# Optimization experiments

Hardware: AMD Instinct MI355X
Metric: run time of the kernel (lower is better)

The kernel has to match this reference:

```python
import jax, jax.numpy as jnp
import numpy as np

G, N, K, H, D = 16, 256, 128, 32, 768
NUM_ATOM_TYPES = 128
NUM_EDGE_TYPES = NUM_ATOM_TYPES * NUM_ATOM_TYPES  # 16384
T_STEPS = 1000


def setup_inputs() -> dict:
    key = jax.random.key(0)
    ks = jax.random.split(key, 12)
    return {
        "pos": jax.random.normal(ks[0], (G, N, 3), dtype=jnp.float32) * 3.0,
        "x": jax.random.randint(ks[1], (G, N, 1), 0, NUM_ATOM_TYPES, dtype=jnp.int32),
        "t": jax.random.randint(ks[2], (G,), 0, T_STEPS, dtype=jnp.int32),
        "means": jax.random.uniform(ks[3], (T_STEPS, K), jnp.float32, 0.0, 3.0),
        "stds": jax.random.uniform(ks[4], (T_STEPS, K), jnp.float32, 0.0, 3.0),
        "mul_w": jnp.ones((NUM_EDGE_TYPES, 1), jnp.float32),
        "bias_w": jnp.zeros((NUM_EDGE_TYPES, 1), jnp.float32),
        "w1": jax.random.normal(ks[5], (K, K), jnp.float32) / np.sqrt(K),
        "b1": jnp.zeros((K,), jnp.float32),
        "w2": jax.random.normal(ks[6], (K, H), jnp.float32) / np.sqrt(K),
        "b2": jnp.zeros((H,), jnp.float32),
        "we": jax.random.normal(ks[7], (K, D), jnp.float32) / np.sqrt(K),
        "be": jnp.zeros((D,), jnp.float32),
    }


def _forward(pos, x, t, means, stds, mul_w, bias_w, w1, b1, w2, b2, we, be):
    atoms = x[:, :, 0]  # [G, N]
    edge_types = atoms[:, :, None] * NUM_ATOM_TYPES + atoms[:, None, :]  # [G,N,N]
    pad = atoms == 0  # [G, N]
    pos = jnp.where(pad[..., None], 0.0, pos)
    # delta_pos[g,i,j] = pos[g,j] - pos[g,i]
    delta_pos = pos[:, None, :, :] - pos[:, :, None, :]  # [G,N,N,3]
    sq = jnp.sum(delta_pos * delta_pos, axis=-1)  # [G,N,N]
    dist = jnp.sqrt(jnp.where(sq > 0, sq, 1.0)) * (sq > 0)  # safe norm, grad-safe at 0
    delta_pos = delta_pos / (dist[..., None] + 1e-5)
    # Gaussian basis expansion
    mul = mul_w[edge_types]   # [G,N,N,1]
    bias = bias_w[edge_types]  # [G,N,N,1]
    xg = mul * dist[..., None] + bias  # [G,N,N,1] -> broadcasts to K
    mean = means[t][:, None, None, :]               # [G,1,1,K]
    std = jnp.abs(stds[t])[:, None, None, :] + 1e-5  # [G,1,1,K]
    a = (2.0 * 3.14159) ** 0.5
    z = (xg - mean) / std
    edge_feature = jnp.exp(-0.5 * z * z) / (a * std)  # [G,N,N,K]
    # NonLinear MLP -> attn bias per head
    h = jax.nn.gelu(edge_feature @ w1 + b1, approximate=False)
    attn_bias = h @ w2 + b2  # [G,N,N,H]
    attn_bias = jnp.transpose(attn_bias, (0, 3, 1, 2))  # [G,H,N,N]
    attn_bias = jnp.where(pad[:, None, None, :], -jnp.inf, attn_bias)
    # masked sum over source nodes + edge projection
    ef = jnp.where(pad[:, None, :, None], 0.0, edge_feature)
    sum_ef = jnp.sum(ef, axis=-2)  # [G,N,K]
    merge = sum_ef @ we + be  # [G,N,D]
    return dist, delta_pos, attn_bias, merge


def reference(pos, x, t, means, stds, mul_w, bias_w, w1, b1, w2, b2, we, be):
    return _forward(pos, x, t, means, stds, mul_w, bias_w, w1, b1, w2, b2, we, be)
```

## Files before the change

### kernel.cpp

```cpp
#include <hip/hip_runtime.h>
#include <hip/hip_bf16.h>
#include <math.h>

#define Gn 16
#define Nn 256
#define Kf 128
#define Hh 32
#define Dd 768
#define NEG_BIG (-3.0e38f)
#define PAD_XG  (1.0e10f)
#define INV_A 0.3989422804014327f
#define NHALF_LOG2E (-0.7213475204444817f)
#define HSIG_A 0.2837f

typedef __attribute__((ext_vector_type(8))) short bf16x8;
typedef __attribute__((ext_vector_type(4))) float f32x4;
typedef __attribute__((ext_vector_type(2))) float f32x2;

static __device__ __forceinline__ float fast_exp2(float x) {
#if __has_builtin(__builtin_amdgcn_exp2f)
    return __builtin_amdgcn_exp2f(x);
#else
    return exp2f(x);
#endif
}

static __device__ __forceinline__ unsigned short f2bf(float f) {
    union { float f; unsigned int u; } v; v.f = f;
    unsigned int r = v.u + 0x7FFF + ((v.u >> 16) & 1);
    return (unsigned short)(r >> 16);
}

__global__ __launch_bounds__(256)
void prep_kernel(const float* __restrict__ w1, const float* __restrict__ w2,
                 const int* __restrict__ tarr, const float* __restrict__ means,
                 const float* __restrict__ stds,
                 unsigned short* __restrict__ w1f, unsigned short* __restrict__ w2f,
                 float4* __restrict__ coef)
{
    const int idx = blockIdx.x * 256 + threadIdx.x;
    if (idx < 2048) {
        const int lane = idx & 63;
        const int nf   = (idx >> 6) & 7;
        const int ks   = idx >> 9;
        const int l15 = lane & 15, lhi = lane >> 4;
        const int n = nf * 16 + l15;
        unsigned short v[8];
#pragma unroll
        for (int e = 0; e < 8; ++e) {
            const int k = ks * 32 + lhi * 8 + e;
            v[e] = f2bf(w1[k * Kf + n]);
        }
        *(uint4*)(w1f + (size_t)idx * 8) = *(const uint4*)v;
    } else if (idx < 2560) {
        const int f2 = idx - 2048;
        const int lane = f2 & 63;
        const int mf   = (f2 >> 6) & 1;
        const int ks   = f2 >> 7;
        const int l15 = lane & 15, lhi = lane >> 4;
        const int m = mf * 16 + l15;
        unsigned short v[8];
#pragma unroll
        for (int e = 0; e < 8; ++e) {
            const int k = ks * 32 + lhi * 8 + e;
            v[e] = f2bf(w2[k * Hh + m]);
        }
        *(uint4*)(w2f + (size_t)f2 * 8) = *(const uint4*)v;
    } else if (idx < 4608) {
        const int e3 = idx - 2560;
        const int g = e3 >> 7, k = e3 & 127;
        const int tg = tarr[g];
        const float mean = means[tg * Kf + k];
        const float sd   = fabsf(stds[tg * Kf + k]) + 1e-5f;
        const float inv  = 1.0f / sd;
        coef[g * Kf + k] =
            make_float4(mean, NHALF_LOG2E * inv * inv, log2f(inv * INV_A), 0.f);
    }
}

__global__ __launch_bounds__(256, 4)
void graph3d_attn_kernel(const float* __restrict__ pos,
                         const int* __restrict__ atoms,
                         const float* __restrict__ mul_w,
                         const float* __restrict__ bias_w,
                         const float* __restrict__ b1,
                         const float* __restrict__ b2,
                         const unsigned short* __restrict__ w1f,
                         const unsigned short* __restrict__ w2f,
                         const float4* __restrict__ coef,
                         float* __restrict__ ws_sum,
                         float* __restrict__ out_dist,
                         float* __restrict__ out_delta,
                         float* __restrict__ out_attn)
{
    const int tid  = threadIdx.x;
    const int half = blockIdx.x;
    const int i    = blockIdx.y;
    const int g    = blockIdx.z;
    const int j0   = half * 128;

    __shared__ __align__(16) unsigned short s_tile[128 * 128];

    const int lane = tid & 63, wq = tid >> 6;
    const int l15 = lane & 15, lhi = lane >> 4;

    if (tid < 128) {
        const int ai = atoms[g * Nn + i];
        float pix = pos[(g * Nn + i) * 3 + 0];
        float piy = pos[(g * Nn + i) * 3 + 1];
        float piz = pos[(g * Nn + i) * 3 + 2];
        if (ai == 0) { pix = 0.f; piy = 0.f; piz = 0.f; }

        const int j  = j0 + tid;
        const int aj = atoms[g * Nn + j];
        float pjx = pos[(g * Nn + j) * 3 + 0];
        float pjy = pos[(g * Nn + j) * 3 + 1];
        float pjz = pos[(g * Nn + j) * 3 + 2];
        if (aj == 0) { pjx = 0.f; pjy = 0.f; pjz = 0.f; }
        const float dx = pjx - pix, dy = pjy - piy, dz = pjz - piz;
        const float sq = dx * dx + dy * dy + dz * dz;
        const float dist = (sq > 0.f) ? sqrtf(sq) : 0.f;
        const float inv_d = 1.f / (dist + 1e-5f);
        const size_t base = (size_t)(g * Nn + i) * Nn + j;
        out_dist[base] = dist;
        out_delta[base * 3 + 0] = dx * inv_d;
        out_delta[base * 3 + 1] = dy * inv_d;
        out_delta[base * 3 + 2] = dz * inv_d;
        const int et = ai * 128 + aj;
        float xg = fmaf(mul_w[et], dist, bias_w[et]);
        if (aj == 0) xg = PAD_XG;
        *(float*)((char*)s_tile + (size_t)((tid >> 5) * 32 + 31) * 256 +
                  (tid & 31) * 4) = xg;
    }
    __syncthreads();

    f32x2 ps = (f32x2){0.f, 0.f};
    {
        const float4 c0 = coef[g * Kf + 2 * lane];
        const float4 c1 = coef[g * Kf + 2 * lane + 1];
        const f32x2 mn = (f32x2){c0.x, c1.x};
        const f32x2 Ak = (f32x2){c0.y, c1.y};
        const f32x2 Ck = (f32x2){c0.z, c1.z};
        char* rowbase = (char*)s_tile + wq * 32 * 256;
        const float* xgp = (const float*)((char*)s_tile + (wq * 32 + 31) * 256);
        const int colb = 4 * lane;
#pragma unroll 8
        for (int jj = 0; jj < 32; ++jj) {
            const float xgj = xgp[jj];
            f32x2 d = (f32x2){xgj, xgj} - mn;
            f32x2 t = Ak * (d * d) + Ck;
            const float e0 = fast_exp2(t.x);
            const float e1 = fast_exp2(t.y);
            ps += (f32x2){e0, e1};
            const __hip_bfloat162 p = __float22bfloat162_rn(make_float2(e0, e1));
            *(unsigned int*)(rowbase + jj * 256 + (colb ^ ((jj & 7) << 4))) =
                *(const unsigned int*)&p;
        }
    }

    const int jrow0 = wq * 32 + l15, jrow1 = jrow0 + 16;
    char* tb0 = (char*)s_tile + jrow0 * 256;
    char* tb1 = (char*)s_tile + jrow1 * 256;
    const int sw0 = (jrow0 & 7) << 4, sw1 = (jrow1 & 7) << 4;
    const unsigned short* w1p = w1f + lane * 8;
    const unsigned short* w2p = w2f + lane * 8;

    f32x4 acc[8][2];
#pragma unroll
    for (int a = 0; a < 8; ++a)
#pragma unroll
        for (int b = 0; b < 2; ++b) acc[a][b] = (f32x4){0.f, 0.f, 0.f, 0.f};

#pragma unroll
    for (int ks = 0; ks < 4; ++ks) {
        const int kb = ks * 64 + lhi * 16;
        const bf16x8 b0  = *(const bf16x8*)(tb0 + (kb ^ sw0));
        const bf16x8 b1f = *(const bf16x8*)(tb1 + (kb ^ sw1));
        bf16x8 a0[4];
#pragma unroll
        for (int nf = 0; nf < 4; ++nf)
            a0[nf] = *(const bf16x8*)(w1p + (ks * 8 + nf) * 512);
#pragma unroll
        for (int nf = 0; nf < 4; ++nf) {
            acc[nf][0] = __builtin_amdgcn_mfma_f32_16x16x32_bf16(a0[nf], b0,  acc[nf][0], 0, 0, 0);
            acc[nf][1] = __builtin_amdgcn_mfma_f32_16x16x32_bf16(a0[nf], b1f, acc[nf][1], 0, 0, 0);
        }
        bf16x8 a1[4];
#pragma unroll
        for (int nf = 0; nf < 4; ++nf)
            a1[nf] = *(const bf16x8*)(w1p + (ks * 8 + nf + 4) * 512);
#pragma unroll
        for (int nf = 0; nf < 4; ++nf) {
            acc[nf + 4][0] = __builtin_amdgcn_mfma_f32_16x16x32_bf16(a1[nf], b0,  acc[nf + 4][0], 0, 0, 0);
            acc[nf + 4][1] = __builtin_amdgcn_mfma_f32_16x16x32_bf16(a1[nf], b1f, acc[nf + 4][1], 0, 0, 0);
        }
    }

#pragma unroll
    for (int nf = 0; nf < 8; ++nf) {
        const float4 bbv = *(const float4*)(b1 + nf * 16 + lhi * 4);
        const f32x4 bb = (f32x4){bbv.x, bbv.y, bbv.z, bbv.w};
        const int colb = 32 * nf + 8 * lhi;
#pragma unroll
        for (int jf = 0; jf < 2; ++jf) {
            char* tb = jf ? tb1 : tb0;
            const int sw = jf ? sw1 : sw0;
            const f32x4 v = acc[nf][jf] + bb;
            f32x4 h;
#pragma unroll
            for (int r = 0; r < 4; ++r) {
                const float s = fminf(fmaxf(fmaf(HSIG_A, v[r], 0.5f), 0.f), 1.f);
                h[r] = v[r] * s;
            }
            const __hip_bfloat162 p0 = __float22bfloat162_rn(make_float2(h.x, h.y));
            const __hip_bfloat162 p1 = __float22bfloat162_rn(make_float2(h.z, h.w));
            uint2 u;
            u.x = *(const unsigned int*)&p0;
            u.y = *(const unsigned int*)&p1;
            *(uint2*)(tb + (colb ^ sw)) = u;
        }
    }

    f32x4 acc2[2][2];
#pragma unroll
    for (int a = 0; a < 2; ++a)
#pragma unroll
        for (int b = 0; b < 2; ++b) acc2[a][b] = (f32x4){0.f, 0.f, 0.f, 0.f};

#pragma unroll
    for (int ks = 0; ks < 4; ++ks) {
        const int kb = ks * 64 + lhi * 16;
        const bf16x8 bh0 = *(const bf16x8*)(tb0 + (kb ^ sw0));
        const bf16x8 bh1 = *(const bf16x8*)(tb1 + (kb ^ sw1));
#pragma unroll
        for (int mf = 0; mf < 2; ++mf) {
            const bf16x8 a2 = *(const bf16x8*)(w2p + (ks * 2 + mf) * 512);
            acc2[mf][0] = __builtin_amdgcn_mfma_f32_16x16x32_bf16(a2, bh0, acc2[mf][0], 0, 0, 0);
            acc2[mf][1] = __builtin_amdgcn_mfma_f32_16x16x32_bf16(a2, bh1, acc2[mf][1], 0, 0, 0);
        }
    }

    __syncthreads();
    {
        float* pt = (float*)s_tile;
        *(f32x2*)&pt[wq * 128 + 2 * lane] = ps;
    }
    __syncthreads();
    if (tid < 128) {
        const float* pt = (const float*)s_tile;
        const float s = (pt[tid] + pt[128 + tid]) + (pt[256 + tid] + pt[384 + tid]);
        ws_sum[((size_t)(g * Nn + i) * 2 + half) * Kf + tid] = s;
    }

    const size_t attn_g = (size_t)g * Hh * (Nn * Nn) + (size_t)i * Nn + j0;
    const float4 b2lo = *(const float4*)(b2 + lhi * 4);
    const float4 b2hi = *(const float4*)(b2 + 16 + lhi * 4);
#pragma unroll
    for (int jf = 0; jf < 2; ++jf) {
        const int jloc = wq * 32 + jf * 16 + l15;
        const bool keep = atoms[g * Nn + j0 + jloc] != 0;
#pragma unroll
        for (int mf = 0; mf < 2; ++mf) {
            const float4 b2v = mf ? b2hi : b2lo;
            const f32x4 v = acc2[mf][jf] + (f32x4){b2v.x, b2v.y, b2v.z, b2v.w};
#pragma unroll
            for (int r = 0; r < 4; ++r) {
                const int m = mf * 16 + lhi * 4 + r;
                out_attn[attn_g + (size_t)m * (Nn * Nn) + jloc] =
                    keep ? v[r] : NEG_BIG;
            }
        }
    }
}

__global__ __launch_bounds__(256)
void graph3d_merge_kernel(const float* __restrict__ ws_sum,
                          const float* __restrict__ we,
                          const float* __restrict__ be,
                          float* __restrict__ out_merge)
{
    const int tid = threadIdx.x;
    const int bd  = blockIdx.x;
    const int r0  = blockIdx.y * 16;
    __shared__ __align__(16) float s_rows[16][128];

#pragma unroll
    for (int p = 0; p < 8; ++p) {
        const int e = p * 256 + tid;
        const int r = e >> 7, k = e & 127;
        const size_t gi = (size_t)(r0 + r);
        s_rows[r][k] = ws_sum[(gi * 2 + 0) * Kf + k] + ws_sum[(gi * 2 + 1) * Kf + k];
    }
    __syncthreads();

    const int col = bd * 256 + tid;
    float acc[16];
#pragma unroll
    for (int r = 0; r < 16; ++r) acc[r] = 0.f;

    for (int k4 = 0; k4 < 32; ++k4) {
        const int k = k4 * 4;
        const float w0  = we[(k + 0) * Dd + col];
        const float w1v = we[(k + 1) * Dd + col];
        const float w2v = we[(k + 2) * Dd + col];
        const float w3  = we[(k + 3) * Dd + col];
#pragma unroll
        for (int r = 0; r < 16; ++r) {
            const float4 s = ((const float4*)&s_rows[r][0])[k4];
            acc[r] = fmaf(s.x, w0, acc[r]);
            acc[r] = fmaf(s.y, w1v, acc[r]);
            acc[r] = fmaf(s.z, w2v, acc[r]);
            acc[r] = fmaf(s.w, w3, acc[r]);
        }
    }

    const float b = be[col];
#pragma unroll
    for (int r = 0; r < 16; ++r)
        out_merge[(size_t)(r0 + r) * Dd + col] = acc[r] + b;
}

extern "C" void kernel_launch(void* const* d_in, const int* in_sizes, int n_in,
                              void* d_out, int out_size, void* d_ws, size_t ws_size,
                              hipStream_t stream) {
    const float* pos    = (const float*)d_in[0];
    const int*   x      = (const int*)  d_in[1];
    const int*   t      = (const int*)  d_in[2];
    const float* means  = (const float*)d_in[3];
    const float* stds   = (const float*)d_in[4];
    const float* mul_w  = (const float*)d_in[5];
    const float* bias_w = (const float*)d_in[6];
    const float* w1     = (const float*)d_in[7];
    const float* b1     = (const float*)d_in[8];
    const float* w2     = (const float*)d_in[9];
    const float* b2     = (const float*)d_in[10];
    const float* we     = (const float*)d_in[11];
    const float* be     = (const float*)d_in[12];

    float* out = (float*)d_out;
    float* out_dist  = out;
    float* out_delta = out + (size_t)Gn * Nn * Nn;
    float* out_attn  = out + (size_t)Gn * Nn * Nn * 4;
    float* out_merge = out + (size_t)Gn * Nn * Nn * 4 + (size_t)Gn * Hh * Nn * Nn;

    float* ws_sum = (float*)d_ws;
    unsigned short* w1f = (unsigned short*)((char*)d_ws + (size_t)Gn * Nn * 2 * Kf * 4);
    unsigned short* w2f = w1f + 2048 * 8;
    float4* coef = (float4*)(w2f + 512 * 8);

    prep_kernel<<<18, 256, 0, stream>>>(w1, w2, t, means, stds, w1f, w2f, coef);

    dim3 gridA(2, Nn, Gn);
    graph3d_attn_kernel<<<gridA, 256, 0, stream>>>(
        pos, x, mul_w, bias_w, b1, b2, w1f, w2f, coef,
        ws_sum, out_dist, out_delta, out_attn);

    dim3 gridB(3, 256);
    graph3d_merge_kernel<<<gridB, 256, 0, stream>>>(
        ws_sum, we, be, out_merge);
}
```

Measured before the change: 113.6 us.

## Remove block barriers via per-wave xg staging and per-wave partial sums

Each wave now computes the xg values for its own 32 rows, which removes the first block-wide barrier. Each wave also writes its own partial Gaussian sums straight to a larger workspace, so the two end-of-kernel barriers and the shared-memory reduction go away. The merge kernel now sums 8 partials instead of 2. The change also adds s_setprio around the MFMA bursts and uses fmed3 for the clamp. The cost is four times more workspace traffic for the partial sums, and position loads are repeated per wave.

```diff
diff --git a/kernel.cpp b/kernel.cpp
--- a/kernel.cpp
+++ b/kernel.cpp
@@ -22,6 +22,13 @@
     return __builtin_amdgcn_exp2f(x);
 #else
     return exp2f(x);
+#endif
+}
+static __device__ __forceinline__ float clamp01(float x) {
+#if __has_builtin(__builtin_amdgcn_fmed3f)
+    return __builtin_amdgcn_fmed3f(x, 0.f, 1.f);
+#else
+    return fminf(fmaxf(x, 0.f), 1.f);
 #endif
 }
 
@@ -104,14 +111,14 @@
     const int lane = tid & 63, wq = tid >> 6;
     const int l15 = lane & 15, lhi = lane >> 4;
 
-    if (tid < 128) {
+    if (lane < 32) {
         const int ai = atoms[g * Nn + i];
         float pix = pos[(g * Nn + i) * 3 + 0];
         float piy = pos[(g * Nn + i) * 3 + 1];
         float piz = pos[(g * Nn + i) * 3 + 2];
         if (ai == 0) { pix = 0.f; piy = 0.f; piz = 0.f; }
 
-        const int j  = j0 + tid;
+        const int j  = j0 + wq * 32 + lane;
         const int aj = atoms[g * Nn + j];
         float pjx = pos[(g * Nn + j) * 3 + 0];
         float pjy = pos[(g * Nn + j) * 3 + 1];
@@ -129,10 +136,8 @@
         const int et = ai * 128 + aj;
         float xg = fmaf(mul_w[et], dist, bias_w[et]);
         if (aj == 0) xg = PAD_XG;
-        *(float*)((char*)s_tile + (size_t)((tid >> 5) * 32 + 31) * 256 +
-                  (tid & 31) * 4) = xg;
-    }
-    __syncthreads();
+        ((float*)((char*)s_tile + (size_t)(wq * 32 + 31) * 256))[lane] = xg;
+    }
 
     f32x2 ps = (f32x2){0.f, 0.f};
     {
@@ -157,6 +162,7 @@
                 *(const unsigned int*)&p;
         }
     }
+    *(f32x2*)&ws_sum[(((size_t)(g * Nn + i) * 2 + half) * 4 + wq) * Kf + 2 * lane] = ps;
 
     const int jrow0 = wq * 32 + l15, jrow1 = jrow0 + 16;
     char* tb0 = (char*)s_tile + jrow0 * 256;
@@ -180,20 +186,24 @@
 #pragma unroll
         for (int nf = 0; nf < 4; ++nf)
             a0[nf] = *(const bf16x8*)(w1p + (ks * 8 + nf) * 512);
+        __builtin_amdgcn_s_setprio(1);
 #pragma unroll
         for (int nf = 0; nf < 4; ++nf) {
             acc[nf][0] = __builtin_amdgcn_mfma_f32_16x16x32_bf16(a0[nf], b0,  acc[nf][0], 0, 0, 0);
             acc[nf][1] = __builtin_amdgcn_mfma_f32_16x16x32_bf16(a0[nf], b1f, acc[nf][1], 0, 0, 0);
         }
+        __builtin_amdgcn_s_setprio(0);
         bf16x8 a1[4];
 #pragma unroll
         for (int nf = 0; nf < 4; ++nf)
             a1[nf] = *(const bf16x8*)(w1p + (ks * 8 + nf + 4) * 512);
+        __builtin_amdgcn_s_setprio(1);
 #pragma unroll
         for (int nf = 0; nf < 4; ++nf) {
             acc[nf + 4][0] = __builtin_amdgcn_mfma_f32_16x16x32_bf16(a1[nf], b0,  acc[nf + 4][0], 0, 0, 0);
             acc[nf + 4][1] = __builtin_amdgcn_mfma_f32_16x16x32_bf16(a1[nf], b1f, acc[nf + 4][1], 0, 0, 0);
         }
+        __builtin_amdgcn_s_setprio(0);
     }
 
 #pragma unroll
@@ -208,10 +218,8 @@
             const f32x4 v = acc[nf][jf] + bb;
             f32x4 h;
 #pragma unroll
-            for (int r = 0; r < 4; ++r) {
-                const float s = fminf(fmaxf(fmaf(HSIG_A, v[r], 0.5f), 0.f), 1.f);
-                h[r] = v[r] * s;
-            }
+            for (int r = 0; r < 4; ++r)
+                h[r] = v[r] * clamp01(fmaf(HSIG_A, v[r], 0.5f));
             const __hip_bfloat162 p0 = __float22bfloat162_rn(make_float2(h.x, h.y));
             const __hip_bfloat162 p1 = __float22bfloat162_rn(make_float2(h.z, h.w));
             uint2 u;
@@ -232,24 +240,14 @@
         const int kb = ks * 64 + lhi * 16;
         const bf16x8 bh0 = *(const bf16x8*)(tb0 + (kb ^ sw0));
         const bf16x8 bh1 = *(const bf16x8*)(tb1 + (kb ^ sw1));
+        __builtin_amdgcn_s_setprio(1);
 #pragma unroll
         for (int mf = 0; mf < 2; ++mf) {
             const bf16x8 a2 = *(const bf16x8*)(w2p + (ks * 2 + mf) * 512);
             acc2[mf][0] = __builtin_amdgcn_mfma_f32_16x16x32_bf16(a2, bh0, acc2[mf][0], 0, 0, 0);
             acc2[mf][1] = __builtin_amdgcn_mfma_f32_16x16x32_bf16(a2, bh1, acc2[mf][1], 0, 0, 0);
         }
-    }
-
-    __syncthreads();
-    {
-        float* pt = (float*)s_tile;
-        *(f32x2*)&pt[wq * 128 + 2 * lane] = ps;
-    }
-    __syncthreads();
-    if (tid < 128) {
-        const float* pt = (const float*)s_tile;
-        const float s = (pt[tid] + pt[128 + tid]) + (pt[256 + tid] + pt[384 + tid]);
-        ws_sum[((size_t)(g * Nn + i) * 2 + half) * Kf + tid] = s;
+        __builtin_amdgcn_s_setprio(0);
     }
 
     const size_t attn_g = (size_t)g * Hh * (Nn * Nn) + (size_t)i * Nn + j0;
@@ -288,8 +286,12 @@
     for (int p = 0; p < 8; ++p) {
         const int e = p * 256 + tid;
         const int r = e >> 7, k = e & 127;
-        const size_t gi = (size_t)(r0 + r);
-        s_rows[r][k] = ws_sum[(gi * 2 + 0) * Kf + k] + ws_sum[(gi * 2 + 1) * Kf + k];
+        const size_t gi = (size_t)(r0 + r) * 8;
+        const float h0 = (ws_sum[(gi + 0) * Kf + k] + ws_sum[(gi + 1) * Kf + k])
+                       + (ws_sum[(gi + 2) * Kf + k] + ws_sum[(gi + 3) * Kf + k]);
+        const float h1 = (ws_sum[(gi + 4) * Kf + k] + ws_sum[(gi + 5) * Kf + k])
+                       + (ws_sum[(gi + 6) * Kf + k] + ws_sum[(gi + 7) * Kf + k]);
+        s_rows[r][k] = h0 + h1;
     }
     __syncthreads();
 
@@ -344,7 +346,7 @@
     float* out_merge = out + (size_t)Gn * Nn * Nn * 4 + (size_t)Gn * Hh * Nn * Nn;
 
     float* ws_sum = (float*)d_ws;
-    unsigned short* w1f = (unsigned short*)((char*)d_ws + (size_t)Gn * Nn * 2 * Kf * 4);
+    unsigned short* w1f = (unsigned short*)((char*)d_ws + (size_t)Gn * Nn * 8 * Kf * 4);
     unsigned short* w2f = w1f + 2048 * 8;
     float4* coef = (float4*)(w2f + 512 * 8);
 
```

Measured after the change: 113.8 us. No clear change (+0.2%).
